# Kernel tuning notes

Measured on AMD Instinct MI355X. Metric: run time of the kernel, lower is better.

Reference implementation:

```python
import jax, jax.numpy as jnp
import numpy as np

EMBED_DIM = 1024
NUM_HEADS = 16
HEAD_DIM = EMBED_DIM // NUM_HEADS
FF_HIDDEN = 4096
ROPE_BASE = 10000.0


def rope(x, start_pos):
    # x: [B, H, S, hd]; interleaved pair rotation
    S, hd = x.shape[2], x.shape[3]
    freqs = 1.0 / ROPE_BASE ** (jnp.arange(0, hd, 2, dtype=jnp.float32) / hd)
    t = jnp.arange(start_pos, start_pos + S, dtype=jnp.float32)
    angles = jnp.outer(t, freqs)            # [S, hd/2]
    cos, sin = jnp.cos(angles), jnp.sin(angles)
    x_even = x[..., 0::2]
    x_odd = x[..., 1::2]
    out_even = x_even * cos - x_odd * sin
    out_odd = x_even * sin + x_odd * cos
    return jnp.stack((out_even, out_odd), axis=-1).reshape(x.shape)


def rmsnorm(x, w, eps=1e-6):
    rms = jnp.sqrt(jnp.mean(x * x, axis=-1, keepdims=True) + eps)
    return x / rms * w


def setup_inputs() -> dict:
    key = jax.random.key(0)
    ks = jax.random.split(key, 8)
    D, H = EMBED_DIM, FF_HIDDEN
    s = lambda fin: 1.0 / np.sqrt(fin)
    return {
        "x": jax.random.normal(ks[0], (2, 2048, D), dtype=jnp.float32),
        "start_pos": 0,
        "norm1_w": jnp.ones((D,), jnp.float32),
        "w_qkv": jax.random.uniform(ks[1], (3 * D, D), jnp.float32, -s(D), s(D)),
        "w_o": jax.random.uniform(ks[2], (D, D), jnp.float32, -s(D), s(D)),
        "norm2_w": jnp.ones((D,), jnp.float32),
        "w_gate": jax.random.uniform(ks[3], (H, D), jnp.float32, -s(D), s(D)),
        "w_up": jax.random.uniform(ks[4], (H, D), jnp.float32, -s(D), s(D)),
        "w_down": jax.random.uniform(ks[5], (D, H), jnp.float32, -s(H), s(H)),
    }


def attention(x, w_qkv, w_o, start_pos):
    B, S, D = x.shape
    qkv = x @ w_qkv.T                         # [B, S, 3D]
    q, k, v = jnp.split(qkv, 3, axis=-1)
    def heads(t):
        return t.reshape(B, S, NUM_HEADS, HEAD_DIM).transpose(0, 2, 1, 3)
    q, k, v = heads(q), heads(k), heads(v)    # [B, H, S, hd]
    q = rope(q, start_pos)
    k = rope(k, start_pos)
    scores = jnp.einsum('bhqd,bhkd->bhqk', q, k) / np.sqrt(HEAD_DIM)
    causal = jnp.tril(jnp.ones((S, S), dtype=bool))
    scores = jnp.where(causal, scores, -jnp.inf)
    attn = jax.nn.softmax(scores, axis=-1)
    out = jnp.einsum('bhqk,bhkd->bhqd', attn, v)
    out = out.transpose(0, 2, 1, 3).reshape(B, S, D)
    return out @ w_o.T


def ffn(x, w_gate, w_up, w_down):
    return (jax.nn.silu(x @ w_gate.T) * (x @ w_up.T)) @ w_down.T


def reference(x, start_pos, norm1_w, w_qkv, w_o, norm2_w, w_gate, w_up, w_down):
    x = x + attention(rmsnorm(x, norm1_w), w_qkv, w_o, start_pos)
    x = x + ffn(rmsnorm(x, norm2_w), w_gate, w_up, w_down)
    return x
```

## Files before the change

kernel.cpp:

```cpp
#include <hip/hip_runtime.h>
#include <math.h>

typedef __bf16 bf16_t;
typedef __bf16 bf16x2 __attribute__((ext_vector_type(2)));
typedef __bf16 bf16x4 __attribute__((ext_vector_type(4)));
typedef __bf16 bf16x8 __attribute__((ext_vector_type(8)));
typedef float f32x4 __attribute__((ext_vector_type(4)));

#define B_ 2
#define S_ 2048
#define D_ 1024
#define NH 16
#define HD 64
#define FF 4096
#define NTOK (B_*S_)

__device__ __forceinline__ f32x4 mfma16(bf16x8 a, bf16x8 b, f32x4 c) {
  return __builtin_amdgcn_mfma_f32_16x16x32_bf16(a, b, c, 0, 0, 0);
}

__device__ __forceinline__ void gld_lds16(const bf16_t* g, bf16_t* l) {
  __builtin_amdgcn_global_load_lds(
      (const __attribute__((address_space(1))) void*)g,
      (__attribute__((address_space(3))) void*)l, 16, 0, 0);
}

__global__ __launch_bounds__(256) void cvt5_kernel(
    const float* __restrict__ p0, const float* __restrict__ p1,
    const float* __restrict__ p2, const float* __restrict__ p3,
    const float* __restrict__ p4,
    bf16_t* __restrict__ o0, bf16_t* __restrict__ o1, bf16_t* __restrict__ o2,
    bf16_t* __restrict__ o3, bf16_t* __restrict__ o4) {
  int i = blockIdx.x * 256 + threadIdx.x;
  const int stride = gridDim.x * 256;
  const int n = 4194304;
  for (; i < n; i += stride) {
    const float* src; bf16_t* dst; int j = i;
    if (j < 786432) { src = p0; dst = o0; }
    else {
      j -= 786432;
      if (j < 262144) { src = p1; dst = o1; }
      else {
        j -= 262144;
        if (j < 1048576) { src = p2; dst = o2; }
        else {
          j -= 1048576;
          if (j < 1048576) { src = p3; dst = o3; }
          else { j -= 1048576; src = p4; dst = o4; }
        }
      }
    }
    float4 v = ((const float4*)src)[j];
    bf16x4 ov;
    ov[0] = (bf16_t)v.x; ov[1] = (bf16_t)v.y; ov[2] = (bf16_t)v.z; ov[3] = (bf16_t)v.w;
    ((bf16x4*)dst)[j] = ov;
  }
}

__global__ __launch_bounds__(256) void rmsnorm_kernel(const float* __restrict__ x,
                                                      const float* __restrict__ w,
                                                      bf16_t* __restrict__ o) {
  const int row = blockIdx.x;
  const float4 v = ((const float4*)(x + (size_t)row * D_))[threadIdx.x];
  float s = v.x*v.x + v.y*v.y + v.z*v.z + v.w*v.w;
  #pragma unroll
  for (int d = 32; d; d >>= 1) s += __shfl_down(s, d);
  __shared__ float acc[4];
  if ((threadIdx.x & 63) == 0) acc[threadIdx.x >> 6] = s;
  __syncthreads();
  const float scale = rsqrtf((acc[0] + acc[1] + acc[2] + acc[3]) * (1.f / D_) + 1e-6f);
  const float4 wv = ((const float4*)w)[threadIdx.x];
  bf16x4 ov;
  ov[0] = (bf16_t)(v.x * scale * wv.x);
  ov[1] = (bf16_t)(v.y * scale * wv.y);
  ov[2] = (bf16_t)(v.z * scale * wv.z);
  ov[3] = (bf16_t)(v.w * scale * wv.w);
  ((bf16x4*)(o + (size_t)row * D_))[threadIdx.x] = ov;
}

template<int MODE, int BN>
__global__ __launch_bounds__(256) void gemm_kernel(
    const bf16_t* __restrict__ A, const bf16_t* __restrict__ W,
    int M, int N, int K,
    float* __restrict__ outF, bf16_t* __restrict__ outB,
    const float* __restrict__ res, const bf16_t* __restrict__ gate) {
  constexpr int NB = BN / 32;
  __shared__ __align__(16) bf16_t lA[2][128 * 32];
  __shared__ __align__(16) bf16_t lB[2][BN * 32];
  const int tid = threadIdx.x;
  const int wave = tid >> 6, lane = tid & 63;
  const int r = lane & 15, kg = lane >> 4;
  const int nx = gridDim.x;
  const int nwg = nx * gridDim.y;
  const int orig = blockIdx.y * nx + blockIdx.x;
  const int q8 = nwg >> 3;
  const int wgid = (orig & 7) * q8 + (orig >> 3);
  const int bm = (wgid / nx) * 128, bn = (wgid % nx) * BN;
  const int wr = (wave >> 1) * 64, wc = (wave & 1) * (BN / 2);
  const bf16_t* Ab = A + (size_t)bm * K;
  const bf16_t* Wb = W + (size_t)bn * K;

  auto stage = [&](int buf, int k0) {
    const int cb0 = (wave << 6);
    const int c0 = cb0 + lane;
    gld_lds16(Ab + (size_t)(c0 >> 2) * K + k0 + (c0 & 3) * 8, lA[buf] + cb0 * 8);
    const int cb1 = cb0 + 256;
    const int c1 = cb1 + lane;
    gld_lds16(Ab + (size_t)(c1 >> 2) * K + k0 + (c1 & 3) * 8, lA[buf] + cb1 * 8);
    gld_lds16(Wb + (size_t)(c0 >> 2) * K + k0 + (c0 & 3) * 8, lB[buf] + cb0 * 8);
    if (BN == 128)
      gld_lds16(Wb + (size_t)(c1 >> 2) * K + k0 + (c1 & 3) * 8, lB[buf] + cb1 * 8);
  };

  f32x4 acc[4][NB] = {};
  stage(0, 0);
  asm volatile("s_waitcnt vmcnt(0)" ::: "memory");
  __syncthreads();
  int cur = 0;
  for (int k0 = 0; k0 < K; k0 += 32) {
    if (k0 + 32 < K) stage(cur ^ 1, k0 + 32);
    const bf16_t* cA = lA[cur];
    const bf16_t* cB = lB[cur];
    bf16x8 af[4], bfr[NB];
    #pragma unroll
    for (int m = 0; m < 4; ++m)
      af[m] = *(const bf16x8*)&cA[(wr + m * 16 + r) * 32 + kg * 8];
    #pragma unroll
    for (int n = 0; n < NB; ++n)
      bfr[n] = *(const bf16x8*)&cB[(wc + n * 16 + r) * 32 + kg * 8];
    #pragma unroll
    for (int m = 0; m < 4; ++m)
      #pragma unroll
      for (int n = 0; n < NB; ++n)
        acc[m][n] = mfma16(af[m], bfr[n], acc[m][n]);
    asm volatile("s_waitcnt vmcnt(0)" ::: "memory");
    __syncthreads();
    cur ^= 1;
  }
  #pragma unroll
  for (int m = 0; m < 4; ++m) {
    const int row0 = bm + wr + m * 16 + kg * 4;
    #pragma unroll
    for (int n = 0; n < NB; ++n) {
      const int col = bn + wc + n * 16 + r;
      #pragma unroll
      for (int g2 = 0; g2 < 4; ++g2) {
        const size_t idx = (size_t)(row0 + g2) * N + col;
        const float v = acc[m][n][g2];
        if (MODE == 0) {
          outB[idx] = (bf16_t)v;
        } else if (MODE == 1) {
          outF[idx] = v + res[idx];
        } else {
          const float gf = (float)gate[idx];
          outB[idx] = (bf16_t)(v * gf / (1.f + __expf(-gf)));
        }
      }
    }
  }
}

__global__ __launch_bounds__(256) void rope_kernel(const bf16_t* __restrict__ qkv,
                                                   bf16_t* __restrict__ q_r,
                                                   bf16_t* __restrict__ k_r,
                                                   const int* __restrict__ start_pos) {
  const int bs = blockIdx.x;
  const int b = bs >> 11, s = bs & (S_ - 1);
  const float t = (float)(s + start_pos[0]);
  const bf16_t* rowp = qkv + (size_t)bs * 3072;
  #pragma unroll
  for (int i = 0; i < 4; ++i) {
    const int p = threadIdx.x + 256 * i;
    const int mat = p >> 9;
    const int rem = p & 511;
    const int h = rem >> 5, d2 = rem & 31;
    const float freq = exp2f((float)d2 * -0.4152410118609203f);
    float sn, cs;
    sincosf(t * freq, &sn, &cs);
    const float qs = mat ? 1.0f : 0.18033688011112042f;
    const bf16x2 e2 = *(const bf16x2*)(rowp + mat * 1024 + h * 64 + 2 * d2);
    const float e = (float)e2[0], od = (float)e2[1];
    bf16x2 ov;
    ov[0] = (bf16_t)((e * cs - od * sn) * qs);
    ov[1] = (bf16_t)((e * sn + od * cs) * qs);
    bf16_t* dst = (mat ? k_r : q_r) + ((size_t)(b * NH + h) * S_ + s) * HD + 2 * d2;
    *(bf16x2*)dst = ov;
  }
}

__global__ __launch_bounds__(256) void vtrans_kernel(const bf16_t* __restrict__ qkv,
                                                     bf16_t* __restrict__ vt) {
  const int bh = blockIdx.y, b = bh >> 4, h = bh & 15;
  const int s0 = blockIdx.x * 64;
  __shared__ bf16_t tile[64][65];
  #pragma unroll
  for (int i = 0; i < 16; ++i) {
    const int idx = threadIdx.x + 256 * i;
    const int sl = idx >> 6, d = idx & 63;
    tile[sl][d] = qkv[(size_t)(b * S_ + s0 + sl) * 3072 + 2048 + h * 64 + d];
  }
  __syncthreads();
  #pragma unroll
  for (int i = 0; i < 16; ++i) {
    const int idx = threadIdx.x + 256 * i;
    const int dl = idx >> 6, sl = idx & 63;
    vt[((size_t)bh * HD + dl) * S_ + s0 + sl] = tile[sl][dl];
  }
}

__global__ __launch_bounds__(256, 4) void attn_kernel(const bf16_t* __restrict__ qr,
                                                      const bf16_t* __restrict__ kr,
                                                      const bf16_t* __restrict__ vt,
                                                      bf16_t* __restrict__ out) {
  const int lid = blockIdx.y * 64 + blockIdx.x;
  const int xcd = lid & 7, slot = lid >> 3;
  const int bh = xcd * 4 + (slot >> 6);
  const int pairIdx = slot & 63;
  const int b = bh >> 4, h = bh & 15;
  const int wave = threadIdx.x >> 6, lane = threadIdx.x & 63;
  const int r = lane & 15, kg = lane >> 4;
  const bf16_t* kb_p = kr + (size_t)bh * S_ * HD;
  const bf16_t* vb_p = vt + (size_t)bh * HD * S_;

  __shared__ __align__(16) f32x4 lo[4][4][64];
  __shared__ float lm[4][64], ll[4][64];

  auto kv_block = [&](int kb, int qbase, const bf16x8& qf0, const bf16x8& qf1,
                      f32x4* o, float& m, float& l, bool masked) {
    f32x4 st[4];
    #pragma unroll
    for (int f = 0; f < 4; ++f) {
      const bf16_t* kp = kb_p + (size_t)(kb + f * 16 + r) * HD;
      f32x4 z = {};
      z = mfma16(*(const bf16x8*)&kp[kg * 8], qf0, z);
      z = mfma16(*(const bf16x8*)&kp[32 + kg * 8], qf1, z);
      st[f] = z;
    }
    float mx = -1e30f;
    #pragma unroll
    for (int f = 0; f < 4; ++f)
      #pragma unroll
      for (int g2 = 0; g2 < 4; ++g2) {
        float v = st[f][g2];
        if (masked) {
          const int k = kb + f * 16 + kg * 4 + g2;
          v = (k <= qbase + r) ? v : -1e30f;
          st[f][g2] = v;
        }
        mx = fmaxf(mx, v);
      }
    mx = fmaxf(mx, __shfl_xor(mx, 16));
    mx = fmaxf(mx, __shfl_xor(mx, 32));
    float alpha = 1.f;
    const bool need = !__all(mx - m <= 8.f);
    if (need) {
      const float nm = fmaxf(m, mx);
      alpha = exp2f(m - nm);
      m = nm;
    }
    float psum = 0.f;
    #pragma unroll
    for (int f = 0; f < 4; ++f)
      #pragma unroll
      for (int g2 = 0; g2 < 4; ++g2) {
        const float p = exp2f(st[f][g2] - m);
        st[f][g2] = p;
        psum += p;
      }
    psum += __shfl_xor(psum, 16);
    psum += __shfl_xor(psum, 32);
    l = l * alpha + psum;
    bf16x8 PA[2];
    #pragma unroll
    for (int fa = 0; fa < 2; ++fa) {
      bf16x8 v;
      #pragma unroll
      for (int j = 0; j < 4; ++j) v[j] = (bf16_t)st[2 * fa][j];
      #pragma unroll
      for (int j = 0; j < 4; ++j) v[4 + j] = (bf16_t)st[2 * fa + 1][j];
      PA[fa] = v;
    }
    if (need) {
      float av[4];
      #pragma unroll
      for (int g2 = 0; g2 < 4; ++g2) av[g2] = __shfl(alpha, kg * 4 + g2);
      #pragma unroll
      for (int dblk = 0; dblk < 4; ++dblk)
        #pragma unroll
        for (int g2 = 0; g2 < 4; ++g2) o[dblk][g2] *= av[g2];
    }
    #pragma unroll
    for (int dblk = 0; dblk < 4; ++dblk) {
      const bf16_t* vp = vb_p + (size_t)(dblk * 16 + r) * S_ + kb;
      #pragma unroll
      for (int fa = 0; fa < 2; ++fa) {
        union { bf16x8 v; bf16x4 hf[2]; } bv;
        bv.hf[0] = *(const bf16x4*)&vp[fa * 32 + kg * 4];
        bv.hf[1] = *(const bf16x4*)&vp[fa * 32 + 16 + kg * 4];
        o[dblk] = mfma16(PA[fa], bv.v, o[dblk]);
      }
    }
  };

  auto run_chunk = [&](int qbase, f32x4* o, float& m, float& l) {
    const bf16_t* qp = qr + ((size_t)bh * S_ + qbase) * HD;
    const bf16x8 qf0 = *(const bf16x8*)&qp[r * HD + kg * 8];
    const bf16x8 qf1 = *(const bf16x8*)&qp[r * HD + 32 + kg * 8];
    int kb = wave * 64;
    for (; kb + 64 <= qbase; kb += 256)
      kv_block(kb, qbase, qf0, qf1, o, m, l, false);
    if (kb < qbase + 16)
      kv_block(kb, qbase, qf0, qf1, o, m, l, true);
  };

  auto store_partial = [&](const f32x4* o, float m, float l) {
    #pragma unroll
    for (int d = 0; d < 4; ++d) lo[wave][d][lane] = o[d];
    lm[wave][lane] = m;
    ll[wave][lane] = l;
  };

  auto merge_write = [&](int qbase) {
    const float ms = fmaxf(fmaxf(lm[0][lane], lm[1][lane]),
                           fmaxf(lm[2][lane], lm[3][lane]));
    float a[4], lt = 0.f;
    #pragma unroll
    for (int i = 0; i < 4; ++i) {
      a[i] = exp2f(lm[i][lane] - ms);
      lt += ll[i][lane] * a[i];
    }
    f32x4 oc = {};
    #pragma unroll
    for (int i = 0; i < 4; ++i) {
      const f32x4 oi = lo[i][wave][lane];
      float av[4];
      #pragma unroll
      for (int g2 = 0; g2 < 4; ++g2) av[g2] = __shfl(a[i], kg * 4 + g2);
      #pragma unroll
      for (int g2 = 0; g2 < 4; ++g2) oc[g2] += oi[g2] * av[g2];
    }
    float lv[4];
    #pragma unroll
    for (int g2 = 0; g2 < 4; ++g2) lv[g2] = __shfl(lt, kg * 4 + g2);
    #pragma unroll
    for (int g2 = 0; g2 < 4; ++g2) {
      const int srow = qbase + kg * 4 + g2;
      out[(size_t)(b * S_ + srow) * D_ + h * HD + wave * 16 + r] =
          (bf16_t)(oc[g2] / lv[g2]);
    }
  };

  {
    const int qbase = pairIdx * 16;
    f32x4 o[4] = {};
    float m = -1e30f, l = 0.f;
    run_chunk(qbase, o, m, l);
    store_partial(o, m, l);
    __syncthreads();
    merge_write(qbase);
    __syncthreads();
  }
  {
    const int qbase = (127 - pairIdx) * 16;
    f32x4 o[4] = {};
    float m = -1e30f, l = 0.f;
    run_chunk(qbase, o, m, l);
    store_partial(o, m, l);
    __syncthreads();
    merge_write(qbase);
  }
}

extern "C" void kernel_launch(void* const* d_in, const int* in_sizes, int n_in,
                              void* d_out, int out_size, void* d_ws, size_t ws_size,
                              hipStream_t stream) {
  const float* x     = (const float*)d_in[0];
  const int*   sp    = (const int*)d_in[1];
  const float* n1w   = (const float*)d_in[2];
  const float* wqkv  = (const float*)d_in[3];
  const float* wo    = (const float*)d_in[4];
  const float* n2w   = (const float*)d_in[5];
  const float* wgate = (const float*)d_in[6];
  const float* wup   = (const float*)d_in[7];
  const float* wdown = (const float*)d_in[8];

  char* p = (char*)d_ws;
  bf16_t* wqkv_b = (bf16_t*)p; p += (size_t)3 * D_ * D_ * 2;
  bf16_t* wo_b   = (bf16_t*)p; p += (size_t)D_ * D_ * 2;
  bf16_t* wg_b   = (bf16_t*)p; p += (size_t)FF * D_ * 2;
  bf16_t* wu_b   = (bf16_t*)p; p += (size_t)FF * D_ * 2;
  bf16_t* wd_b   = (bf16_t*)p; p += (size_t)FF * D_ * 2;
  bf16_t* xn     = (bf16_t*)p; p += (size_t)NTOK * D_ * 2;
  float*  x1     = (float*)p;  p += (size_t)NTOK * D_ * 4;
  char* pool = p;
  bf16_t* qkv    = (bf16_t*)(pool);
  bf16_t* q_r    = (bf16_t*)(pool + (size_t)25165824);
  bf16_t* k_r    = (bf16_t*)(pool + (size_t)33554432);
  bf16_t* v_t    = (bf16_t*)(pool + (size_t)41943040);
  bf16_t* attn_o = (bf16_t*)(pool + (size_t)50331648);
  bf16_t* gbuf   = (bf16_t*)(pool);
  bf16_t* hbuf   = (bf16_t*)(pool + (size_t)33554432);

  cvt5_kernel<<<dim3(2048), dim3(256), 0, stream>>>(
      wqkv, wo, wgate, wup, wdown, wqkv_b, wo_b, wg_b, wu_b, wd_b);

  rmsnorm_kernel<<<dim3(NTOK), dim3(256), 0, stream>>>(x, n1w, xn);

  gemm_kernel<0,128><<<dim3(3 * D_ / 128, NTOK / 128), dim3(256), 0, stream>>>(
      xn, wqkv_b, NTOK, 3 * D_, D_, nullptr, qkv, nullptr, nullptr);

  rope_kernel<<<dim3(NTOK), dim3(256), 0, stream>>>(qkv, q_r, k_r, sp);
  vtrans_kernel<<<dim3(S_ / 64, B_ * NH), dim3(256), 0, stream>>>(qkv, v_t);

  attn_kernel<<<dim3(64, B_ * NH), dim3(256), 0, stream>>>(q_r, k_r, v_t, attn_o);

  gemm_kernel<1,64><<<dim3(D_ / 64, NTOK / 128), dim3(256), 0, stream>>>(
      attn_o, wo_b, NTOK, D_, D_, x1, nullptr, x, nullptr);

  rmsnorm_kernel<<<dim3(NTOK), dim3(256), 0, stream>>>(x1, n2w, xn);

  gemm_kernel<0,128><<<dim3(FF / 128, NTOK / 128), dim3(256), 0, stream>>>(
      xn, wg_b, NTOK, FF, D_, nullptr, gbuf, nullptr, nullptr);

  gemm_kernel<2,128><<<dim3(FF / 128, NTOK / 128), dim3(256), 0, stream>>>(
      xn, wu_b, NTOK, FF, D_, nullptr, hbuf, nullptr, gbuf);

  gemm_kernel<1,64><<<dim3(D_ / 64, NTOK / 128), dim3(256), 0, stream>>>(
      hbuf, wd_b, NTOK, D_, FF, (float*)d_out, nullptr, x1, nullptr);
}
```

Baseline: 561.1 us.

## Software-pipeline K/V register loads in attention kernel and relax occupancy bound

Restructures the attention inner loop so K fragments for the next KV block are prefetched into registers while the current block's QK^T and softmax run. V is loaded at the start of each iteration, ahead of the PV MFMAs. Launch bounds drop from 4 to 2 blocks per CU so the extra prefetch registers fit. The aim is to hide global-load latency, at the cost of lower occupancy and higher register pressure.

Result: no change. 564.9 us (+0.7%).

```diff
diff --git a/kernel.cpp b/kernel.cpp
--- a/kernel.cpp
+++ b/kernel.cpp
@@ -208,7 +208,7 @@
   }
 }
 
-__global__ __launch_bounds__(256, 4) void attn_kernel(const bf16_t* __restrict__ qr,
+__global__ __launch_bounds__(256, 2) void attn_kernel(const bf16_t* __restrict__ qr,
                                                       const bf16_t* __restrict__ kr,
                                                       const bf16_t* __restrict__ vt,
                                                       bf16_t* __restrict__ out) {
@@ -225,70 +225,15 @@
   __shared__ __align__(16) f32x4 lo[4][4][64];
   __shared__ float lm[4][64], ll[4][64];
 
-  auto kv_block = [&](int kb, int qbase, const bf16x8& qf0, const bf16x8& qf1,
-                      f32x4* o, float& m, float& l, bool masked) {
-    f32x4 st[4];
+  auto load_K = [&](int kb, bf16x8* kf) {
     #pragma unroll
     for (int f = 0; f < 4; ++f) {
       const bf16_t* kp = kb_p + (size_t)(kb + f * 16 + r) * HD;
-      f32x4 z = {};
-      z = mfma16(*(const bf16x8*)&kp[kg * 8], qf0, z);
-      z = mfma16(*(const bf16x8*)&kp[32 + kg * 8], qf1, z);
-      st[f] = z;
-    }
-    float mx = -1e30f;
-    #pragma unroll
-    for (int f = 0; f < 4; ++f)
-      #pragma unroll
-      for (int g2 = 0; g2 < 4; ++g2) {
-        float v = st[f][g2];
-        if (masked) {
-          const int k = kb + f * 16 + kg * 4 + g2;
-          v = (k <= qbase + r) ? v : -1e30f;
-          st[f][g2] = v;
-        }
-        mx = fmaxf(mx, v);
-      }
-    mx = fmaxf(mx, __shfl_xor(mx, 16));
-    mx = fmaxf(mx, __shfl_xor(mx, 32));
-    float alpha = 1.f;
-    const bool need = !__all(mx - m <= 8.f);
-    if (need) {
-      const float nm = fmaxf(m, mx);
-      alpha = exp2f(m - nm);
-      m = nm;
-    }
-    float psum = 0.f;
-    #pragma unroll
-    for (int f = 0; f < 4; ++f)
-      #pragma unroll
-      for (int g2 = 0; g2 < 4; ++g2) {
-        const float p = exp2f(st[f][g2] - m);
-        st[f][g2] = p;
-        psum += p;
-      }
-    psum += __shfl_xor(psum, 16);
-    psum += __shfl_xor(psum, 32);
-    l = l * alpha + psum;
-    bf16x8 PA[2];
-    #pragma unroll
-    for (int fa = 0; fa < 2; ++fa) {
-      bf16x8 v;
-      #pragma unroll
-      for (int j = 0; j < 4; ++j) v[j] = (bf16_t)st[2 * fa][j];
-      #pragma unroll
-      for (int j = 0; j < 4; ++j) v[4 + j] = (bf16_t)st[2 * fa + 1][j];
-      PA[fa] = v;
-    }
-    if (need) {
-      float av[4];
-      #pragma unroll
-      for (int g2 = 0; g2 < 4; ++g2) av[g2] = __shfl(alpha, kg * 4 + g2);
-      #pragma unroll
-      for (int dblk = 0; dblk < 4; ++dblk)
-        #pragma unroll
-        for (int g2 = 0; g2 < 4; ++g2) o[dblk][g2] *= av[g2];
-    }
+      kf[2 * f]     = *(const bf16x8*)&kp[kg * 8];
+      kf[2 * f + 1] = *(const bf16x8*)&kp[32 + kg * 8];
+    }
+  };
+  auto load_V = [&](int kb, bf16x8* vf) {
     #pragma unroll
     for (int dblk = 0; dblk < 4; ++dblk) {
       const bf16_t* vp = vb_p + (size_t)(dblk * 16 + r) * S_ + kb;
@@ -297,20 +242,96 @@
         union { bf16x8 v; bf16x4 hf[2]; } bv;
         bv.hf[0] = *(const bf16x4*)&vp[fa * 32 + kg * 4];
         bv.hf[1] = *(const bf16x4*)&vp[fa * 32 + 16 + kg * 4];
-        o[dblk] = mfma16(PA[fa], bv.v, o[dblk]);
+        vf[dblk * 2 + fa] = bv.v;
       }
     }
   };
 
   auto run_chunk = [&](int qbase, f32x4* o, float& m, float& l) {
+    if (wave * 64 >= qbase + 16) return;
     const bf16_t* qp = qr + ((size_t)bh * S_ + qbase) * HD;
     const bf16x8 qf0 = *(const bf16x8*)&qp[r * HD + kg * 8];
     const bf16x8 qf1 = *(const bf16x8*)&qp[r * HD + 32 + kg * 8];
     int kb = wave * 64;
-    for (; kb + 64 <= qbase; kb += 256)
-      kv_block(kb, qbase, qf0, qf1, o, m, l, false);
-    if (kb < qbase + 16)
-      kv_block(kb, qbase, qf0, qf1, o, m, l, true);
+    bf16x8 kcur[8], knxt[8], vcur[8];
+    load_K(kb, kcur);
+    while (true) {
+      const bool cur_masked = (kb + 64 > qbase);
+      const int kb2 = kb + 256;
+      const bool has_next = (kb2 < qbase + 16);
+      load_V(kb, vcur);
+      f32x4 st[4];
+      #pragma unroll
+      for (int f = 0; f < 4; ++f) {
+        f32x4 z = {};
+        z = mfma16(kcur[2 * f], qf0, z);
+        z = mfma16(kcur[2 * f + 1], qf1, z);
+        st[f] = z;
+      }
+      if (has_next) load_K(kb2, knxt);
+      float mx = -1e30f;
+      #pragma unroll
+      for (int f = 0; f < 4; ++f)
+        #pragma unroll
+        for (int g2 = 0; g2 < 4; ++g2) {
+          float v = st[f][g2];
+          if (cur_masked) {
+            const int k = kb + f * 16 + kg * 4 + g2;
+            v = (k <= qbase + r) ? v : -1e30f;
+            st[f][g2] = v;
+          }
+          mx = fmaxf(mx, v);
+        }
+      mx = fmaxf(mx, __shfl_xor(mx, 16));
+      mx = fmaxf(mx, __shfl_xor(mx, 32));
+      float alpha = 1.f;
+      const bool need = !__all(mx - m <= 8.f);
+      if (need) {
+        const float nm = fmaxf(m, mx);
+        alpha = exp2f(m - nm);
+        m = nm;
+      }
+      float psum = 0.f;
+      #pragma unroll
+      for (int f = 0; f < 4; ++f)
+        #pragma unroll
+        for (int g2 = 0; g2 < 4; ++g2) {
+          const float p = exp2f(st[f][g2] - m);
+          st[f][g2] = p;
+          psum += p;
+        }
+      psum += __shfl_xor(psum, 16);
+      psum += __shfl_xor(psum, 32);
+      l = l * alpha + psum;
+      bf16x8 PA[2];
+      #pragma unroll
+      for (int fa = 0; fa < 2; ++fa) {
+        bf16x8 v;
+        #pragma unroll
+        for (int j = 0; j < 4; ++j) v[j] = (bf16_t)st[2 * fa][j];
+        #pragma unroll
+        for (int j = 0; j < 4; ++j) v[4 + j] = (bf16_t)st[2 * fa + 1][j];
+        PA[fa] = v;
+      }
+      if (need) {
+        float av[4];
+        #pragma unroll
+        for (int g2 = 0; g2 < 4; ++g2) av[g2] = __shfl(alpha, kg * 4 + g2);
+        #pragma unroll
+        for (int dblk = 0; dblk < 4; ++dblk)
+          #pragma unroll
+          for (int g2 = 0; g2 < 4; ++g2) o[dblk][g2] *= av[g2];
+      }
+      #pragma unroll
+      for (int dblk = 0; dblk < 4; ++dblk) {
+        o[dblk] = mfma16(PA[0], vcur[dblk * 2], o[dblk]);
+        o[dblk] = mfma16(PA[1], vcur[dblk * 2 + 1], o[dblk]);
+      }
+      if (!has_next) break;
+      #pragma unroll
+      for (int i = 0; i < 8; ++i) kcur[i] = knxt[i];
+      kb = kb2;
+    }
   };
 
   auto store_partial = [&](const f32x4* o, float m, float l) {
```
